# Performance work log

Measured on AMD Instinct MI355X. Metric: run time of the kernel, lower is better.

## Reference

```python
import jax, jax.numpy as jnp
import numpy as np

N, D, H, E, K, C = 8192, 1024, 2048, 8, 2, 2560  # tokens, d_model, hidden, experts, top_k, capacity


def setup_inputs() -> dict:
    key = jax.random.key(0)
    ks = jax.random.split(key, 8)
    s_in, s_h = 1.0 / np.sqrt(D), 1.0 / np.sqrt(H)
    return {
        "x": jax.random.normal(ks[0], (N, D), jnp.float32),
        "Wg": jax.random.uniform(ks[1], (D, E), jnp.float32, -s_in, s_in),
        "bg": jnp.zeros((E,), jnp.float32),
        "W1": jax.random.uniform(ks[2], (E, D, H), jnp.float32, -s_in, s_in),
        "b1": jnp.zeros((E, H), jnp.float32),
        "W2": jax.random.uniform(ks[3], (E, H, H), jnp.float32, -s_h, s_h),
        "b2": jnp.zeros((E, H), jnp.float32),
    }


def reference(x, Wg, bg, W1, b1, W2, b2):
    n = x.shape[0]
    logits = x @ Wg + bg                                  # [N, E]
    probs = jax.nn.softmax(logits, axis=-1)
    topk_probs, topk_idx = jax.lax.top_k(probs, K)        # [N, K]

    # auxiliary losses (training mode)
    importance = probs.sum(0)
    importance_loss = jnp.var(importance) / (E ** 2)
    rows = jnp.arange(n)[:, None]
    mask = jnp.zeros_like(probs).at[rows, topk_idx].set(1.0)
    routing_probs = probs * mask
    expert_usage = mask.mean(0)
    routing_weights = routing_probs.mean(0)
    load_balance_loss = E * (expert_usage * routing_weights).sum()
    aux_loss = importance_loss + load_balance_loss

    # dispatch: rank of each (token, k) slot within its expert, in flat order
    flat_e = topk_idx.reshape(-1)                          # [N*K]
    flat_p = topk_probs.reshape(-1)                        # [N*K]
    sample_idx = jnp.repeat(jnp.arange(n), K)              # [N*K]
    oh = (flat_e[:, None] == jnp.arange(E)[None, :]).astype(jnp.int32)  # [N*K, E]
    rank = jnp.take_along_axis(jnp.cumsum(oh, axis=0), flat_e[:, None], axis=1)[:, 0] - 1
    keep = rank < C                                        # capacity truncation (first-come)
    r_safe = jnp.where(keep, rank, C)                      # C is out-of-bounds -> dropped

    buf = jnp.zeros((E, C, D), x.dtype).at[flat_e, r_safe].set(x[sample_idx], mode="drop")
    h = jax.nn.gelu(jnp.einsum("ecd,edh->ech", buf, W1) + b1[:, None, :], approximate=False)
    y = jnp.einsum("ech,eho->eco", h, W2) + b2[:, None, :]  # [E, C, H]

    gathered = y[flat_e, jnp.minimum(r_safe, C - 1)]       # [N*K, H]
    weighted = gathered * (flat_p * keep.astype(x.dtype))[:, None]
    outputs = jnp.zeros((n, H), x.dtype).at[sample_idx].add(weighted)
    return outputs, aux_loss
```

## Files before the change

### kernel.cpp

```cpp
#include <hip/hip_runtime.h>
#include <math.h>
#include <stdint.h>

#define N_TOK 8192
#define DMODEL 1024
#define HID 2048
#define NEXP 8
#define TOPK 2
#define CAP 2560

typedef __bf16 bf16x8 __attribute__((ext_vector_type(8)));
typedef float f32x4 __attribute__((ext_vector_type(4)));

__device__ __forceinline__ unsigned short f2b(float f) {
    unsigned int u = __builtin_bit_cast(unsigned int, f);
    u += 0x7fffu + ((u >> 16) & 1u);
    return (unsigned short)(u >> 16);
}
__device__ __forceinline__ float b2f(unsigned short s) {
    unsigned int u = ((unsigned int)s) << 16;
    return __builtin_bit_cast(float, u);
}

__device__ __forceinline__ void gload_lds16(const void* g, void* lds) {
    __builtin_amdgcn_global_load_lds(
        (const __attribute__((address_space(1))) unsigned int*)(uintptr_t)g,
        (__attribute__((address_space(3))) unsigned int*)(unsigned int)(uintptr_t)lds,
        16, 0, 0);
}

__global__ __launch_bounds__(256) void gate_kernel(
    const float* __restrict__ x, const float* __restrict__ Wg,
    const float* __restrict__ bg,
    int* __restrict__ flat_e, float* __restrict__ flat_p,
    float* __restrict__ imp_part, float* __restrict__ sel_part)
{
    __shared__ float s_imp[4][NEXP];
    __shared__ float s_sel[4][NEXP];
    const int wave = threadIdx.x >> 6;
    const int lane = threadIdx.x & 63;
    const int t = blockIdx.x * 4 + wave;

    float acc[NEXP];
#pragma unroll
    for (int e = 0; e < NEXP; ++e) acc[e] = 0.f;
    const float* xr = x + (size_t)t * DMODEL;
    for (int d = lane; d < DMODEL; d += 64) {
        const float xv = xr[d];
#pragma unroll
        for (int e = 0; e < NEXP; ++e) acc[e] += xv * Wg[d * NEXP + e];
    }
#pragma unroll
    for (int off = 32; off > 0; off >>= 1) {
#pragma unroll
        for (int e = 0; e < NEXP; ++e) acc[e] += __shfl_xor(acc[e], off);
    }
    float lg[NEXP], mx = -1e30f;
#pragma unroll
    for (int e = 0; e < NEXP; ++e) { lg[e] = acc[e] + bg[e]; mx = fmaxf(mx, lg[e]); }
    float p[NEXP], s = 0.f;
#pragma unroll
    for (int e = 0; e < NEXP; ++e) { p[e] = expf(lg[e] - mx); s += p[e]; }
    const float inv = 1.f / s;
#pragma unroll
    for (int e = 0; e < NEXP; ++e) p[e] *= inv;

    int i0 = 0;
#pragma unroll
    for (int e = 1; e < NEXP; ++e) if (p[e] > p[i0]) i0 = e;
    int i1 = (i0 == 0) ? 1 : 0;
#pragma unroll
    for (int e = 0; e < NEXP; ++e) if (e != i0 && p[e] > p[i1]) i1 = e;

    if (lane == 0) {
        flat_e[2 * t] = i0;  flat_e[2 * t + 1] = i1;
        flat_p[2 * t] = p[i0]; flat_p[2 * t + 1] = p[i1];
#pragma unroll
        for (int e = 0; e < NEXP; ++e) {
            s_imp[wave][e] = p[e];
            s_sel[wave][e] = (e == i0) ? p[i0] : ((e == i1) ? p[i1] : 0.f);
        }
    }
    __syncthreads();
    if (threadIdx.x < NEXP) {
        const int e = threadIdx.x;
        float a = 0.f, b = 0.f;
#pragma unroll
        for (int w = 0; w < 4; ++w) { a += s_imp[w][e]; b += s_sel[w][e]; }
        imp_part[blockIdx.x * NEXP + e] = a;
        sel_part[blockIdx.x * NEXP + e] = b;
    }
}

__global__ __launch_bounds__(1024) void scan_kernel(
    const int* __restrict__ flat_e, int* __restrict__ slot_rank,
    int* __restrict__ row_token, int* __restrict__ n_kept,
    int* __restrict__ cnt_full)
{
    __shared__ int wave_tot[16][NEXP];
    __shared__ int base[NEXP];
    const int tid = threadIdx.x, lane = tid & 63, w = tid >> 6;
    if (tid < NEXP) base[tid] = 0;
    __syncthreads();
    const unsigned long long ltmask =
        (lane == 0) ? 0ull : (~0ull >> (64 - lane));
    for (int chunk = 0; chunk < (N_TOK * TOPK) / 1024; ++chunk) {
        const int s = chunk * 1024 + tid;
        const int e = flat_e[s];
        int prefix = 0;
#pragma unroll
        for (int ee = 0; ee < NEXP; ++ee) {
            unsigned long long m = __ballot(e == ee);
            if (ee == e) prefix = __popcll(m & ltmask);
            if (lane == 0) wave_tot[w][ee] = __popcll(m);
        }
        __syncthreads();
        int before = base[e];
        for (int ww = 0; ww < w; ++ww) before += wave_tot[ww][e];
        const int rank = before + prefix;
        slot_rank[s] = rank;
        if (rank < CAP) row_token[e * CAP + rank] = s >> 1;
        __syncthreads();
        if (tid < NEXP) {
            int add = 0;
#pragma unroll
            for (int ww = 0; ww < 16; ++ww) add += wave_tot[ww][tid];
            base[tid] += add;
        }
        __syncthreads();
    }
    for (int i = tid; i < NEXP * CAP; i += 1024) {
        const int ee = i / CAP;
        const int r = i - ee * CAP;
        const int ne = base[ee] < CAP ? base[ee] : CAP;
        if (r >= ne) row_token[i] = N_TOK;
    }
    if (tid < NEXP) {
        n_kept[tid] = min(base[tid], CAP);
        cnt_full[tid] = base[tid];
    }
}

__global__ __launch_bounds__(256) void convert_x(
    const float* __restrict__ x, unsigned short* __restrict__ xbf)
{
    const size_t i = ((size_t)blockIdx.x * 256 + threadIdx.x) * 4;
    float4 v = make_float4(0.f, 0.f, 0.f, 0.f);
    if (i < (size_t)N_TOK * DMODEL) v = *(const float4*)(x + i);
    ushort4 o;
    o.x = f2b(v.x); o.y = f2b(v.y); o.z = f2b(v.z); o.w = f2b(v.w);
    *(ushort4*)(xbf + i) = o;
}

__global__ __launch_bounds__(256) void transpose_cvt(
    const float* __restrict__ W, unsigned short* __restrict__ Wt,
    const int R, const int Cdim)
{
    __shared__ unsigned short s[64][66];
    const int e = blockIdx.z;
    const int c0 = blockIdx.x * 64, r0 = blockIdx.y * 64;
    const float* We = W + (size_t)e * R * Cdim;
    unsigned short* Wte = Wt + (size_t)e * R * Cdim;
    const int lr = threadIdx.x >> 6;
    const int lc = threadIdx.x & 63;
#pragma unroll
    for (int i = 0; i < 16; ++i)
        s[lr + i * 4][lc] = f2b(We[(size_t)(r0 + lr + i * 4) * Cdim + c0 + lc]);
    __syncthreads();
#pragma unroll
    for (int i = 0; i < 16; ++i)
        Wte[(size_t)(c0 + lr + i * 4) * R + r0 + lc] = s[lc][lr + i * 4];
}

#define VMGATE() do { asm volatile("s_waitcnt vmcnt(4)" ::: "memory"); \
                      __builtin_amdgcn_sched_barrier(0); } while (0)
#define NOGATE() ((void)0)

#define PHASE(mf0, STAGE_STMT, TAIL_STMT) do {                                   \
    bf16x8 a0 = lda(c, (mf0), 0), a1 = lda(c, (mf0), 1);                         \
    bf16x8 a2 = lda(c, (mf0) + 1, 0), a3 = lda(c, (mf0) + 1, 1);                 \
    STAGE_STMT;                                                                  \
    __builtin_amdgcn_s_barrier();                                                \
    asm volatile("s_waitcnt lgkmcnt(0)" ::: "memory");                           \
    __builtin_amdgcn_sched_barrier(0);                                           \
    __builtin_amdgcn_s_setprio(1);                                               \
    _Pragma("unroll")                                                            \
    for (int nf = 0; nf < 4; ++nf) {                                             \
        acc[(mf0)][nf] = __builtin_amdgcn_mfma_f32_16x16x32_bf16(                \
            a0, bfr[nf][0], acc[(mf0)][nf], 0, 0, 0);                            \
        acc[(mf0)][nf] = __builtin_amdgcn_mfma_f32_16x16x32_bf16(                \
            a1, bfr[nf][1], acc[(mf0)][nf], 0, 0, 0);                            \
        acc[(mf0) + 1][nf] = __builtin_amdgcn_mfma_f32_16x16x32_bf16(            \
            a2, bfr[nf][0], acc[(mf0) + 1][nf], 0, 0, 0);                        \
        acc[(mf0) + 1][nf] = __builtin_amdgcn_mfma_f32_16x16x32_bf16(            \
            a3, bfr[nf][1], acc[(mf0) + 1][nf], 0, 0, 0);                        \
    }                                                                            \
    __builtin_amdgcn_s_setprio(0);                                               \
    TAIL_STMT;                                                                   \
    __builtin_amdgcn_s_barrier();                                                \
} while (0)

template <bool GATHER, bool DO_GELU>
__global__ __launch_bounds__(512, 2) void mfma_gemm256(
    const unsigned short* __restrict__ A,
    const unsigned short* __restrict__ Wt,
    const float* __restrict__ bias,
    unsigned short* __restrict__ out,
    const int* __restrict__ row_token, const int* __restrict__ n_kept,
    const int Kdim)
{
    __shared__ unsigned short smem[65536];

    int bid = blockIdx.x;
    const int cpx = gridDim.x >> 3;
    bid = (bid & 7) * cpx + (bid >> 3);
    const int e = bid / 80;
    const int rem = bid - e * 80;
    const int m0 = (rem >> 3) * 256;
    const int n0 = (rem & 7) * 256;

    const int n_e = n_kept[e];
    if (m0 >= n_e) return;

    const int t = threadIdx.x;
    const int w = t >> 6, lane = t & 63;
    const int wm = w >> 2, wn = w & 3;
    const int l15 = lane & 15, lq = lane >> 4;

    long abase[2][2], bbase[2][2];
#pragma unroll
    for (int h = 0; h < 2; ++h) {
#pragma unroll
        for (int cc = 0; cc < 2; ++cc) {
            const int srow = h * 128 + cc * 64 + (t >> 3);
            const int skoff = ((t & 7) * 8) ^ ((srow & 4) << 2);
            long ar;
            if (GATHER) ar = (long)row_token[e * CAP + m0 + srow] * Kdim;
            else        ar = ((long)e * CAP + m0 + srow) * (long)Kdim;
            abase[h][cc] = ar + skoff;
            bbase[h][cc] = ((long)e * HID + n0 + srow) * (long)Kdim + skoff;
        }
    }

    auto stageA = [&](int buf, int h0, int ktile) {
        const long ko = (long)ktile * 64;
        char* base = (char*)smem + buf * 32768 + h0 * 16384 + w * 1024;
        gload_lds16(A + (h0 ? abase[1][0] : abase[0][0]) + ko, base);
        gload_lds16(A + (h0 ? abase[1][1] : abase[0][1]) + ko, base + 8192);
    };
    auto stageB = [&](int buf, int h0, int ktile) {
        const long ko = (long)ktile * 64;
        char* base = (char*)smem + 65536 + buf * 32768 + h0 * 16384 + w * 1024;
        gload_lds16(Wt + (h0 ? bbase[1][0] : bbase[0][0]) + ko, base);
        gload_lds16(Wt + (h0 ? bbase[1][1] : bbase[0][1]) + ko, base + 8192);
    };

    const int sx = (l15 & 4) << 3;
    const int kbx0 = (lq * 16) ^ sx;
    const int kbx1 = (64 + lq * 16) ^ sx;
    auto lda = [&](int cbuf, int mf, int ks) -> bf16x8 {
        return *(const bf16x8*)((const char*)smem + cbuf * 32768 +
                                (wm * 128 + mf * 16 + l15) * 128 + (ks ? kbx1 : kbx0));
    };
    auto ldb = [&](int cbuf, int nf, int ks) -> bf16x8 {
        return *(const bf16x8*)((const char*)smem + 65536 + cbuf * 32768 +
                                (wn * 64 + nf * 16 + l15) * 128 + (ks ? kbx1 : kbx0));
    };

    f32x4 acc[8][4];
#pragma unroll
    for (int m = 0; m < 8; ++m)
#pragma unroll
        for (int n = 0; n < 4; ++n) acc[m][n] = (f32x4)0.f;

    const int NT = Kdim >> 6;

    stageA(0, 0, 0); stageA(0, 1, 0);
    stageB(0, 0, 0); stageB(0, 1, 0);
    stageB(1, 0, 1); stageB(1, 1, 1);
    VMGATE();
    __builtin_amdgcn_s_barrier();

    for (int kt = 0; kt < NT; ++kt) {
        const int c = kt & 1, o = c ^ 1;
        const int ktA = min(kt + 1, NT - 1);
        const int ktB = min(kt + 2, NT - 1);

        bf16x8 bfr[4][2];
#pragma unroll
        for (int nf = 0; nf < 4; ++nf) {
            bfr[nf][0] = ldb(c, nf, 0);
            bfr[nf][1] = ldb(c, nf, 1);
        }
        PHASE(0, stageA(o, 0, ktA), NOGATE());
        PHASE(2, stageA(o, 1, ktA), NOGATE());
        PHASE(4, stageB(c, 0, ktB), NOGATE());
        PHASE(6, stageB(c, 1, ktB), VMGATE());
    }

    const float* be = bias + (size_t)e * HID;
    float bv[4];
#pragma unroll
    for (int nf = 0; nf < 4; ++nf)
        bv[nf] = be[n0 + wn * 64 + nf * 16 + l15];
#pragma unroll
    for (int mf = 0; mf < 8; ++mf) {
#pragma unroll
        for (int j = 0; j < 4; ++j) {
            const int row = m0 + wm * 128 + mf * 16 + lq * 4 + j;
            unsigned short* orow =
                out + ((size_t)e * CAP + row) * HID + n0 + wn * 64 + l15;
#pragma unroll
            for (int nf = 0; nf < 4; ++nf) {
                float v = acc[mf][nf][j] + bv[nf];
                if (DO_GELU) v = 0.5f * v * (1.f + erff(v * 0.70710678118654752440f));
                orow[nf * 16] = f2b(v);
            }
        }
    }
}

__global__ __launch_bounds__(256) void combine_kernel(
    const unsigned short* __restrict__ y, const int* __restrict__ flat_e,
    const float* __restrict__ flat_p, const int* __restrict__ slot_rank,
    float* __restrict__ out)
{
    const int t = blockIdx.x;
    const int e0 = flat_e[2 * t], e1 = flat_e[2 * t + 1];
    const int r0 = slot_rank[2 * t], r1 = slot_rank[2 * t + 1];
    const bool k0 = r0 < CAP, k1 = r1 < CAP;
    const float w0 = k0 ? flat_p[2 * t] : 0.f;
    const float w1 = k1 ? flat_p[2 * t + 1] : 0.f;
    const unsigned short* y0 = y + ((size_t)e0 * CAP + (k0 ? r0 : 0)) * HID;
    const unsigned short* y1 = y + ((size_t)e1 * CAP + (k1 ? r1 : 0)) * HID;
    float* orow = out + (size_t)t * HID;
    const int c = threadIdx.x * 8;
    uint4 av = k0 ? *(const uint4*)(y0 + c) : make_uint4(0, 0, 0, 0);
    uint4 bv = k1 ? *(const uint4*)(y1 + c) : make_uint4(0, 0, 0, 0);
    float o[8];
    auto comb2 = [&](unsigned int a, unsigned int b, float* dst) {
        dst[0] = w0 * b2f((unsigned short)(a & 0xffffu)) +
                 w1 * b2f((unsigned short)(b & 0xffffu));
        dst[1] = w0 * b2f((unsigned short)(a >> 16)) +
                 w1 * b2f((unsigned short)(b >> 16));
    };
    comb2(av.x, bv.x, o + 0); comb2(av.y, bv.y, o + 2);
    comb2(av.z, bv.z, o + 4); comb2(av.w, bv.w, o + 6);
    *(float4*)(orow + c)     = make_float4(o[0], o[1], o[2], o[3]);
    *(float4*)(orow + c + 4) = make_float4(o[4], o[5], o[6], o[7]);
}

__global__ __launch_bounds__(64) void aux_kernel(
    const float* __restrict__ imp_part, const float* __restrict__ sel_part,
    const int* __restrict__ cnt_full, float* __restrict__ out_aux,
    const int nparts)
{
    const int lane = threadIdx.x;
    __shared__ float imp_s[NEXP], sel_s[NEXP];
    for (int e = 0; e < NEXP; ++e) {
        float a = 0.f, b = 0.f;
        for (int i = lane; i < nparts; i += 64) {
            a += imp_part[i * NEXP + e];
            b += sel_part[i * NEXP + e];
        }
#pragma unroll
        for (int off = 32; off > 0; off >>= 1) {
            a += __shfl_xor(a, off);
            b += __shfl_xor(b, off);
        }
        if (lane == 0) { imp_s[e] = a; sel_s[e] = b; }
    }
    __syncthreads();
    if (lane == 0) {
        double mean = 0.0;
        for (int e = 0; e < NEXP; ++e) mean += imp_s[e];
        mean /= NEXP;
        double var = 0.0;
        for (int e = 0; e < NEXP; ++e) {
            const double d = (double)imp_s[e] - mean;
            var += d * d;
        }
        var /= NEXP;
        double load = 0.0;
        for (int e = 0; e < NEXP; ++e)
            load += ((double)cnt_full[e] / N_TOK) * ((double)sel_s[e] / N_TOK);
        load *= NEXP;
        out_aux[0] = (float)(var / (NEXP * NEXP) + load);
    }
}

extern "C" void kernel_launch(void* const* d_in, const int* in_sizes, int n_in,
                              void* d_out, int out_size, void* d_ws, size_t ws_size,
                              hipStream_t stream) {
    const float* x  = (const float*)d_in[0];
    const float* Wg = (const float*)d_in[1];
    const float* bg = (const float*)d_in[2];
    const float* W1 = (const float*)d_in[3];
    const float* b1 = (const float*)d_in[4];
    const float* W2 = (const float*)d_in[5];
    const float* b2 = (const float*)d_in[6];
    float* out = (float*)d_out;
    (void)in_sizes; (void)n_in; (void)out_size; (void)ws_size;

    char* ws = (char*)d_ws;
    size_t off = 0;
    auto alloc = [&](size_t bytes) -> void* {
        void* p = ws + off;
        off = (off + bytes + 255) & ~(size_t)255;
        return p;
    };
    int*   n_kept    = (int*)alloc(NEXP * sizeof(int));
    int*   cnt_full  = (int*)alloc(NEXP * sizeof(int));
    int*   flat_e    = (int*)alloc((size_t)N_TOK * TOPK * sizeof(int));
    float* flat_p    = (float*)alloc((size_t)N_TOK * TOPK * sizeof(float));
    int*   slot_rank = (int*)alloc((size_t)N_TOK * TOPK * sizeof(int));
    int*   row_tok   = (int*)alloc((size_t)NEXP * CAP * sizeof(int));
    float* imp_part  = (float*)alloc((size_t)(N_TOK / 4) * NEXP * sizeof(float));
    float* sel_part  = (float*)alloc((size_t)(N_TOK / 4) * NEXP * sizeof(float));
    unsigned short* xbf  = (unsigned short*)alloc((size_t)(N_TOK + 1) * DMODEL * 2);
    unsigned short* w1t  = (unsigned short*)alloc((size_t)NEXP * DMODEL * HID * 2);
    unsigned short* w2t  = (unsigned short*)alloc((size_t)NEXP * HID * HID * 2);
    unsigned short* hbuf = (unsigned short*)alloc((size_t)NEXP * CAP * HID * 2);
    unsigned short* ybuf = (unsigned short*)alloc((size_t)NEXP * CAP * HID * 2);

    convert_x<<<(N_TOK + 1) * DMODEL / 1024, 256, 0, stream>>>(x, xbf);
    transpose_cvt<<<dim3(HID / 64, DMODEL / 64, NEXP), 256, 0, stream>>>(W1, w1t, DMODEL, HID);
    transpose_cvt<<<dim3(HID / 64, HID / 64, NEXP), 256, 0, stream>>>(W2, w2t, HID, HID);

    gate_kernel<<<N_TOK / 4, 256, 0, stream>>>(x, Wg, bg, flat_e, flat_p,
                                               imp_part, sel_part);
    scan_kernel<<<1, 1024, 0, stream>>>(flat_e, slot_rank, row_tok, n_kept, cnt_full);

    const int nblk = NEXP * (CAP / 256) * (HID / 256);
    mfma_gemm256<true,  true ><<<nblk, 512, 0, stream>>>(xbf,  w1t, b1, hbuf, row_tok, n_kept, DMODEL);
    mfma_gemm256<false, false><<<nblk, 512, 0, stream>>>(hbuf, w2t, b2, ybuf, row_tok, n_kept, HID);

    combine_kernel<<<N_TOK, 256, 0, stream>>>(ybuf, flat_e, flat_p, slot_rank, out);
    aux_kernel<<<1, 64, 0, stream>>>(imp_part, sel_part, cnt_full,
                                     out + (size_t)N_TOK * HID, N_TOK / 4);
}
```

Measured before the change: 534.5 us.

## Pre-gather tokens per expert, stage GEMM epilogue through LDS, approximate GELU

Replaces the full-x bf16 conversion with a pack kernel that gathers only routed tokens into a contiguous per-expert bf16 buffer, so the first GEMM no longer does indirect row addressing. The GEMM epilogue now writes results through LDS and stores coalesced 16-byte rows instead of scattered 2-byte stores. GELU uses an Abramowitz-Stegun erf polynomial with fast reciprocal and exp instead of erff. The weight transpose also packs 8 bf16 per store. The erf approximation adds error of roughly 1e-7 absolute on top of the bf16 rounding.

```diff
diff --git a/kernel.cpp b/kernel.cpp
--- a/kernel.cpp
+++ b/kernel.cpp
@@ -20,6 +20,16 @@
 __device__ __forceinline__ float b2f(unsigned short s) {
     unsigned int u = ((unsigned int)s) << 16;
     return __builtin_bit_cast(float, u);
+}
+
+__device__ __forceinline__ float gelu_f(float v) {
+    const float ax = fabsf(v) * 0.70710678118654752440f;
+    const float t = __builtin_amdgcn_rcpf(1.f + 0.3275911f * ax);
+    float poly = ((((1.061405429f * t - 1.453152027f) * t + 1.421413741f) * t
+                   - 0.284496736f) * t + 0.254829592f) * t;
+    float er = 1.f - poly * __expf(-ax * ax);
+    er = (v >= 0.f) ? er : -er;
+    return 0.5f * v * (1.f + er);
 }
 
 __device__ __forceinline__ void gload_lds16(const void* g, void* lds) {
@@ -141,15 +151,27 @@
     }
 }
 
-__global__ __launch_bounds__(256) void convert_x(
-    const float* __restrict__ x, unsigned short* __restrict__ xbf)
-{
-    const size_t i = ((size_t)blockIdx.x * 256 + threadIdx.x) * 4;
-    float4 v = make_float4(0.f, 0.f, 0.f, 0.f);
-    if (i < (size_t)N_TOK * DMODEL) v = *(const float4*)(x + i);
-    ushort4 o;
-    o.x = f2b(v.x); o.y = f2b(v.y); o.z = f2b(v.z); o.w = f2b(v.w);
-    *(ushort4*)(xbf + i) = o;
+__global__ __launch_bounds__(256) void pack_a(
+    const float* __restrict__ x, const int* __restrict__ row_token,
+    unsigned short* __restrict__ xg)
+{
+    const int w = threadIdx.x >> 6, lane = threadIdx.x & 63;
+    const int r = blockIdx.x * 4 + w;
+    const int tok = row_token[r];
+    unsigned short* orow = xg + (size_t)r * DMODEL;
+    if (tok >= N_TOK) {
+#pragma unroll
+        for (int i = 0; i < 4; ++i)
+            *(ushort4*)(orow + i * 256 + lane * 4) = make_ushort4(0, 0, 0, 0);
+        return;
+    }
+    const float* xr = x + (size_t)tok * DMODEL;
+#pragma unroll
+    for (int i = 0; i < 4; ++i) {
+        float4 v = *(const float4*)(xr + i * 256 + lane * 4);
+        *(ushort4*)(orow + i * 256 + lane * 4) =
+            make_ushort4(f2b(v.x), f2b(v.y), f2b(v.z), f2b(v.w));
+    }
 }
 
 __global__ __launch_bounds__(256) void transpose_cvt(
@@ -161,15 +183,25 @@
     const int c0 = blockIdx.x * 64, r0 = blockIdx.y * 64;
     const float* We = W + (size_t)e * R * Cdim;
     unsigned short* Wte = Wt + (size_t)e * R * Cdim;
-    const int lr = threadIdx.x >> 6;
-    const int lc = threadIdx.x & 63;
+    const int tid = threadIdx.x;
+    const int lr = tid >> 6;
+    const int lc = tid & 63;
 #pragma unroll
     for (int i = 0; i < 16; ++i)
         s[lr + i * 4][lc] = f2b(We[(size_t)(r0 + lr + i * 4) * Cdim + c0 + lc]);
     __syncthreads();
 #pragma unroll
-    for (int i = 0; i < 16; ++i)
-        Wte[(size_t)(c0 + lr + i * 4) * R + r0 + lc] = s[lc][lr + i * 4];
+    for (int pass = 0; pass < 2; ++pass) {
+        const int cc = (tid >> 3) + pass * 32;
+        const int rq = (tid & 7) * 8;
+        unsigned short v[8];
+#pragma unroll
+        for (int k = 0; k < 8; ++k) v[k] = s[rq + k][cc];
+        uint4 o;
+        o.x = v[0] | ((unsigned)v[1] << 16); o.y = v[2] | ((unsigned)v[3] << 16);
+        o.z = v[4] | ((unsigned)v[5] << 16); o.w = v[6] | ((unsigned)v[7] << 16);
+        *(uint4*)&Wte[(size_t)(c0 + cc) * R + r0 + rq] = o;
+    }
 }
 
 #define VMGATE() do { asm volatile("s_waitcnt vmcnt(4)" ::: "memory"); \
@@ -200,13 +232,13 @@
     __builtin_amdgcn_s_barrier();                                                \
 } while (0)
 
-template <bool GATHER, bool DO_GELU>
+template <bool DO_GELU>
 __global__ __launch_bounds__(512, 2) void mfma_gemm256(
     const unsigned short* __restrict__ A,
     const unsigned short* __restrict__ Wt,
     const float* __restrict__ bias,
     unsigned short* __restrict__ out,
-    const int* __restrict__ row_token, const int* __restrict__ n_kept,
+    const int* __restrict__ n_kept,
     const int Kdim)
 {
     __shared__ unsigned short smem[65536];
@@ -234,10 +266,7 @@
         for (int cc = 0; cc < 2; ++cc) {
             const int srow = h * 128 + cc * 64 + (t >> 3);
             const int skoff = ((t & 7) * 8) ^ ((srow & 4) << 2);
-            long ar;
-            if (GATHER) ar = (long)row_token[e * CAP + m0 + srow] * Kdim;
-            else        ar = ((long)e * CAP + m0 + srow) * (long)Kdim;
-            abase[h][cc] = ar + skoff;
+            abase[h][cc] = ((long)e * CAP + m0 + srow) * (long)Kdim + skoff;
             bbase[h][cc] = ((long)e * HID + n0 + srow) * (long)Kdim + skoff;
         }
     }
@@ -303,20 +332,41 @@
 #pragma unroll
     for (int nf = 0; nf < 4; ++nf)
         bv[nf] = be[n0 + wn * 64 + nf * 16 + l15];
-#pragma unroll
-    for (int mf = 0; mf < 8; ++mf) {
-#pragma unroll
-        for (int j = 0; j < 4; ++j) {
-            const int row = m0 + wm * 128 + mf * 16 + lq * 4 + j;
-            unsigned short* orow =
-                out + ((size_t)e * CAP + row) * HID + n0 + wn * 64 + l15;
-#pragma unroll
-            for (int nf = 0; nf < 4; ++nf) {
-                float v = acc[mf][nf][j] + bv[nf];
-                if (DO_GELU) v = 0.5f * v * (1.f + erff(v * 0.70710678118654752440f));
-                orow[nf * 16] = f2b(v);
-            }
-        }
+
+    __syncthreads();
+    float* sl = (float*)smem;
+    for (int mf0 = 0; mf0 < 8; mf0 += 2) {
+#pragma unroll
+        for (int mfL = 0; mfL < 2; ++mfL)
+#pragma unroll
+            for (int nf = 0; nf < 4; ++nf)
+#pragma unroll
+                for (int j = 0; j < 4; ++j) {
+                    float v = acc[mf0 + mfL][nf][j] + bv[nf];
+                    if (DO_GELU) v = gelu_f(v);
+                    const int r = mfL * 32 + wm * 16 + lq * 4 + j;
+                    sl[r * 260 + wn * 64 + nf * 16 + l15] = v;
+                }
+        __syncthreads();
+#pragma unroll
+        for (int q = 0; q < 4; ++q) {
+            const int u = q * 512 + t;
+            const int r = u >> 5;
+            const int cg = (u & 31) * 8;
+            const float* p = &sl[r * 260 + cg];
+            float4 v0 = *(const float4*)p, v1 = *(const float4*)(p + 4);
+            uint4 ov;
+            ov.x = f2b(v0.x) | ((unsigned)f2b(v0.y) << 16);
+            ov.y = f2b(v0.z) | ((unsigned)f2b(v0.w) << 16);
+            ov.z = f2b(v1.x) | ((unsigned)f2b(v1.y) << 16);
+            ov.w = f2b(v1.z) | ((unsigned)f2b(v1.w) << 16);
+            const int mfL2 = r >> 5;
+            const int wmr = (r >> 4) & 1;
+            const int rl = r & 15;
+            const int grow = m0 + wmr * 128 + (mf0 + mfL2) * 16 + rl;
+            *(uint4*)(out + ((size_t)e * CAP + grow) * HID + n0 + cg) = ov;
+        }
+        __syncthreads();
     }
 }
 
@@ -417,23 +467,23 @@
     int*   row_tok   = (int*)alloc((size_t)NEXP * CAP * sizeof(int));
     float* imp_part  = (float*)alloc((size_t)(N_TOK / 4) * NEXP * sizeof(float));
     float* sel_part  = (float*)alloc((size_t)(N_TOK / 4) * NEXP * sizeof(float));
-    unsigned short* xbf  = (unsigned short*)alloc((size_t)(N_TOK + 1) * DMODEL * 2);
+    unsigned short* xg   = (unsigned short*)alloc((size_t)NEXP * CAP * DMODEL * 2);
     unsigned short* w1t  = (unsigned short*)alloc((size_t)NEXP * DMODEL * HID * 2);
     unsigned short* w2t  = (unsigned short*)alloc((size_t)NEXP * HID * HID * 2);
     unsigned short* hbuf = (unsigned short*)alloc((size_t)NEXP * CAP * HID * 2);
     unsigned short* ybuf = (unsigned short*)alloc((size_t)NEXP * CAP * HID * 2);
 
-    convert_x<<<(N_TOK + 1) * DMODEL / 1024, 256, 0, stream>>>(x, xbf);
     transpose_cvt<<<dim3(HID / 64, DMODEL / 64, NEXP), 256, 0, stream>>>(W1, w1t, DMODEL, HID);
     transpose_cvt<<<dim3(HID / 64, HID / 64, NEXP), 256, 0, stream>>>(W2, w2t, HID, HID);
 
     gate_kernel<<<N_TOK / 4, 256, 0, stream>>>(x, Wg, bg, flat_e, flat_p,
                                                imp_part, sel_part);
     scan_kernel<<<1, 1024, 0, stream>>>(flat_e, slot_rank, row_tok, n_kept, cnt_full);
+    pack_a<<<NEXP * CAP / 4, 256, 0, stream>>>(x, row_tok, xg);
 
     const int nblk = NEXP * (CAP / 256) * (HID / 256);
-    mfma_gemm256<true,  true ><<<nblk, 512, 0, stream>>>(xbf,  w1t, b1, hbuf, row_tok, n_kept, DMODEL);
-    mfma_gemm256<false, false><<<nblk, 512, 0, stream>>>(hbuf, w2t, b2, ybuf, row_tok, n_kept, HID);
+    mfma_gemm256<true ><<<nblk, 512, 0, stream>>>(xg,   w1t, b1, hbuf, n_kept, DMODEL);
+    mfma_gemm256<false><<<nblk, 512, 0, stream>>>(hbuf, w2t, b2, ybuf, n_kept, HID);
 
     combine_kernel<<<N_TOK, 256, 0, stream>>>(ybuf, flat_e, flat_p, slot_rank, out);
     aux_kernel<<<1, 64, 0, stream>>>(imp_part, sel_part, cnt_full,
```

Result: slower. 568.0 us (+6.3%).

## Triple-buffer B tiles, use polynomial GELU, vectorize transpose stores, add nontemporal memory ops

Applied to the files above, without the earlier changes.

Several independent changes land together. The GEMM B operand moves to a triple-buffered LDS ring, which raises shared memory to 160KB, and the loop stops issuing redundant clamped loads on the last iterations, draining with vmcnt(0) at the end. GELU now uses the Abramowitz-Stegun erf polynomial with a hardware reciprocal and fast exp instead of erff, which lowers accuracy slightly. The transpose kernel writes 16-byte packed stores with nontemporal loads, the combine kernel and the second GEMM's output use nontemporal memory ops, and each weight transpose is launched right before the GEMM that consumes it. The larger LDS footprint may prevent two blocks per CU from being resident.

```diff
diff --git a/kernel.cpp b/kernel.cpp
--- a/kernel.cpp
+++ b/kernel.cpp
@@ -11,6 +11,7 @@
 
 typedef __bf16 bf16x8 __attribute__((ext_vector_type(8)));
 typedef float f32x4 __attribute__((ext_vector_type(4)));
+typedef unsigned int u32x4 __attribute__((ext_vector_type(4)));
 
 __device__ __forceinline__ unsigned short f2b(float f) {
     unsigned int u = __builtin_bit_cast(unsigned int, f);
@@ -20,6 +21,16 @@
 __device__ __forceinline__ float b2f(unsigned short s) {
     unsigned int u = ((unsigned int)s) << 16;
     return __builtin_bit_cast(float, u);
+}
+
+__device__ __forceinline__ float gelu_f(float v) {
+    const float ax = fabsf(v) * 0.70710678118654752440f;
+    const float t = __builtin_amdgcn_rcpf(1.f + 0.3275911f * ax);
+    float poly = ((((1.061405429f * t - 1.453152027f) * t + 1.421413741f) * t
+                   - 0.284496736f) * t + 0.254829592f) * t;
+    float er = 1.f - poly * __expf(-ax * ax);
+    er = (v >= 0.f) ? er : -er;
+    return 0.5f * v * (1.f + er);
 }
 
 __device__ __forceinline__ void gload_lds16(const void* g, void* lds) {
@@ -161,19 +172,32 @@
     const int c0 = blockIdx.x * 64, r0 = blockIdx.y * 64;
     const float* We = W + (size_t)e * R * Cdim;
     unsigned short* Wte = Wt + (size_t)e * R * Cdim;
-    const int lr = threadIdx.x >> 6;
-    const int lc = threadIdx.x & 63;
+    const int tid = threadIdx.x;
+    const int lr = tid >> 6;
+    const int lc = tid & 63;
 #pragma unroll
     for (int i = 0; i < 16; ++i)
-        s[lr + i * 4][lc] = f2b(We[(size_t)(r0 + lr + i * 4) * Cdim + c0 + lc]);
+        s[lr + i * 4][lc] =
+            f2b(__builtin_nontemporal_load(&We[(size_t)(r0 + lr + i * 4) * Cdim + c0 + lc]));
     __syncthreads();
 #pragma unroll
-    for (int i = 0; i < 16; ++i)
-        Wte[(size_t)(c0 + lr + i * 4) * R + r0 + lc] = s[lc][lr + i * 4];
-}
-
-#define VMGATE() do { asm volatile("s_waitcnt vmcnt(4)" ::: "memory"); \
-                      __builtin_amdgcn_sched_barrier(0); } while (0)
+    for (int pass = 0; pass < 2; ++pass) {
+        const int cc = (tid >> 3) + pass * 32;
+        const int rq = (tid & 7) * 8;
+        unsigned short v[8];
+#pragma unroll
+        for (int k = 0; k < 8; ++k) v[k] = s[rq + k][cc];
+        u32x4 o;
+        o[0] = v[0] | ((unsigned)v[1] << 16); o[1] = v[2] | ((unsigned)v[3] << 16);
+        o[2] = v[4] | ((unsigned)v[5] << 16); o[3] = v[6] | ((unsigned)v[7] << 16);
+        *(u32x4*)&Wte[(size_t)(c0 + cc) * R + r0 + rq] = o;
+    }
+}
+
+#define VMGATE4() do { asm volatile("s_waitcnt vmcnt(4)" ::: "memory"); \
+                       __builtin_amdgcn_sched_barrier(0); } while (0)
+#define VMGATE0() do { asm volatile("s_waitcnt vmcnt(0)" ::: "memory"); \
+                       __builtin_amdgcn_sched_barrier(0); } while (0)
 #define NOGATE() ((void)0)
 
 #define PHASE(mf0, STAGE_STMT, TAIL_STMT) do {                                   \
@@ -200,7 +224,7 @@
     __builtin_amdgcn_s_barrier();                                                \
 } while (0)
 
-template <bool GATHER, bool DO_GELU>
+template <bool GATHER, bool DO_GELU, bool NT_OUT>
 __global__ __launch_bounds__(512, 2) void mfma_gemm256(
     const unsigned short* __restrict__ A,
     const unsigned short* __restrict__ Wt,
@@ -209,7 +233,7 @@
     const int* __restrict__ row_token, const int* __restrict__ n_kept,
     const int Kdim)
 {
-    __shared__ unsigned short smem[65536];
+    __shared__ unsigned short smem[81920];
 
     int bid = blockIdx.x;
     const int cpx = gridDim.x >> 3;
@@ -278,24 +302,31 @@
     stageA(0, 0, 0); stageA(0, 1, 0);
     stageB(0, 0, 0); stageB(0, 1, 0);
     stageB(1, 0, 1); stageB(1, 1, 1);
-    VMGATE();
+    VMGATE4();
     __builtin_amdgcn_s_barrier();
 
+    int bcur = 0;
     for (int kt = 0; kt < NT; ++kt) {
         const int c = kt & 1, o = c ^ 1;
-        const int ktA = min(kt + 1, NT - 1);
-        const int ktB = min(kt + 2, NT - 1);
+        const int ktA = kt + 1;
+        const int ktB = kt + 2;
+        int bst = bcur + 2; if (bst >= 3) bst -= 3;
 
         bf16x8 bfr[4][2];
 #pragma unroll
         for (int nf = 0; nf < 4; ++nf) {
-            bfr[nf][0] = ldb(c, nf, 0);
-            bfr[nf][1] = ldb(c, nf, 1);
-        }
-        PHASE(0, stageA(o, 0, ktA), NOGATE());
-        PHASE(2, stageA(o, 1, ktA), NOGATE());
-        PHASE(4, stageB(c, 0, ktB), NOGATE());
-        PHASE(6, stageB(c, 1, ktB), VMGATE());
+            bfr[nf][0] = ldb(bcur, nf, 0);
+            bfr[nf][1] = ldb(bcur, nf, 1);
+        }
+        PHASE(0, if (ktA < NT) stageA(o, 0, ktA), NOGATE());
+        PHASE(2, if (ktA < NT) stageA(o, 1, ktA), NOGATE());
+        PHASE(4, if (ktB < NT) stageB(bst, 0, ktB), NOGATE());
+        if (ktB < NT) {
+            PHASE(6, stageB(bst, 1, ktB), VMGATE4());
+        } else {
+            PHASE(6, NOGATE(), VMGATE0());
+        }
+        bcur = (bcur == 2) ? 0 : bcur + 1;
     }
 
     const float* be = bias + (size_t)e * HID;
@@ -313,8 +344,9 @@
 #pragma unroll
             for (int nf = 0; nf < 4; ++nf) {
                 float v = acc[mf][nf][j] + bv[nf];
-                if (DO_GELU) v = 0.5f * v * (1.f + erff(v * 0.70710678118654752440f));
-                orow[nf * 16] = f2b(v);
+                if (DO_GELU) v = gelu_f(v);
+                if (NT_OUT) __builtin_nontemporal_store(f2b(v), &orow[nf * 16]);
+                else        orow[nf * 16] = f2b(v);
             }
         }
     }
@@ -335,8 +367,8 @@
     const unsigned short* y1 = y + ((size_t)e1 * CAP + (k1 ? r1 : 0)) * HID;
     float* orow = out + (size_t)t * HID;
     const int c = threadIdx.x * 8;
-    uint4 av = k0 ? *(const uint4*)(y0 + c) : make_uint4(0, 0, 0, 0);
-    uint4 bv = k1 ? *(const uint4*)(y1 + c) : make_uint4(0, 0, 0, 0);
+    u32x4 av = k0 ? __builtin_nontemporal_load((const u32x4*)(y0 + c)) : (u32x4)0u;
+    u32x4 bv = k1 ? __builtin_nontemporal_load((const u32x4*)(y1 + c)) : (u32x4)0u;
     float o[8];
     auto comb2 = [&](unsigned int a, unsigned int b, float* dst) {
         dst[0] = w0 * b2f((unsigned short)(a & 0xffffu)) +
@@ -344,10 +376,12 @@
         dst[1] = w0 * b2f((unsigned short)(a >> 16)) +
                  w1 * b2f((unsigned short)(b >> 16));
     };
-    comb2(av.x, bv.x, o + 0); comb2(av.y, bv.y, o + 2);
-    comb2(av.z, bv.z, o + 4); comb2(av.w, bv.w, o + 6);
-    *(float4*)(orow + c)     = make_float4(o[0], o[1], o[2], o[3]);
-    *(float4*)(orow + c + 4) = make_float4(o[4], o[5], o[6], o[7]);
+    comb2(av[0], bv[0], o + 0); comb2(av[1], bv[1], o + 2);
+    comb2(av[2], bv[2], o + 4); comb2(av[3], bv[3], o + 6);
+    f32x4 o0 = {o[0], o[1], o[2], o[3]};
+    f32x4 o1 = {o[4], o[5], o[6], o[7]};
+    __builtin_nontemporal_store(o0, (f32x4*)(orow + c));
+    __builtin_nontemporal_store(o1, (f32x4*)(orow + c + 4));
 }
 
 __global__ __launch_bounds__(64) void aux_kernel(
@@ -424,16 +458,19 @@
     unsigned short* ybuf = (unsigned short*)alloc((size_t)NEXP * CAP * HID * 2);
 
     convert_x<<<(N_TOK + 1) * DMODEL / 1024, 256, 0, stream>>>(x, xbf);
-    transpose_cvt<<<dim3(HID / 64, DMODEL / 64, NEXP), 256, 0, stream>>>(W1, w1t, DMODEL, HID);
-    transpose_cvt<<<dim3(HID / 64, HID / 64, NEXP), 256, 0, stream>>>(W2, w2t, HID, HID);
-
     gate_kernel<<<N_TOK / 4, 256, 0, stream>>>(x, Wg, bg, flat_e, flat_p,
                                                imp_part, sel_part);
     scan_kernel<<<1, 1024, 0, stream>>>(flat_e, slot_rank, row_tok, n_kept, cnt_full);
 
     const int nblk = NEXP * (CAP / 256) * (HID / 256);
-    mfma_gemm256<true,  true ><<<nblk, 512, 0, stream>>>(xbf,  w1t, b1, hbuf, row_tok, n_kept, DMODEL);
-    mfma_gemm256<false, false><<<nblk, 512, 0, stream>>>(hbuf, w2t, b2, ybuf, row_tok, n_kept, HID);
+
+    transpose_cvt<<<dim3(HID / 64, DMODEL / 64, NEXP), 256, 0, stream>>>(W1, w1t, DMODEL, HID);
+    mfma_gemm256<true,  true,  false><<<nblk, 512, 0, stream>>>(
+        xbf,  w1t, b1, hbuf, row_tok, n_kept, DMODEL);
+
+    transpose_cvt<<<dim3(HID / 64, HID / 64, NEXP), 256, 0, stream>>>(W2, w2t, HID, HID);
+    mfma_gemm256<false, false, true ><<<nblk, 512, 0, stream>>>(
+        hbuf, w2t, b2, ybuf, row_tok, n_kept, HID);
 
     combine_kernel<<<N_TOK, 256, 0, stream>>>(ybuf, flat_e, flat_p, slot_rank, out);
     aux_kernel<<<1, 64, 0, stream>>>(imp_part, sel_part, cnt_full,
```

New measurement: 488.1 us. -8.7%, faster.
